# Optimization experiments

Hardware: AMD Instinct MI355X
Metric: run time of the kernel (lower is better)

## Reference

```python
import jax, jax.numpy as jnp
import numpy as np

IN_F = 4096
OUT_F = 4096
N = 16384


def setup_inputs() -> dict:
    key = jax.random.key(0)
    ks = jax.random.split(key, 7)
    return {
        "x": jax.random.normal(ks[0], (N, IN_F), dtype=jnp.float32),
        "weight_mu": jax.random.normal(ks[1], (OUT_F, IN_F), dtype=jnp.float32) * 0.1,
        "weight_rho": jax.random.normal(ks[2], (OUT_F, IN_F), dtype=jnp.float32) * 0.1,
        "bias_mu": jax.random.normal(ks[3], (OUT_F,), dtype=jnp.float32) * 0.1,
        "bias_rho": jax.random.normal(ks[4], (OUT_F,), dtype=jnp.float32) * 0.1,
        "eps_w": jax.random.normal(ks[5], (OUT_F, IN_F), dtype=jnp.float32),
        "eps_b": jax.random.normal(ks[6], (OUT_F,), dtype=jnp.float32),
    }


def reference(x, weight_mu, weight_rho, bias_mu, bias_rho, eps_w, eps_b):
    # softplus: log(1 + exp(rho)), written as log1p(exp(.)) for stability
    weight = weight_mu + jnp.log1p(jnp.exp(weight_rho)) * eps_w  # [out, in]
    bias = bias_mu + jnp.log1p(jnp.exp(bias_rho)) * eps_b        # [out]
    # F.linear(x, W, b) = x @ W.T + b
    return jnp.einsum("ni,oi->no", x, weight) + bias
```

## Files before the change

kernel.cpp:

```cpp
#include <hip/hip_runtime.h>
#include <hip/hip_bf16.h>

typedef unsigned short u16;
typedef __attribute__((ext_vector_type(4))) float f32x4;
typedef __attribute__((ext_vector_type(8))) short bf16x8;

__device__ __forceinline__ u16 f2bf(float f) {
    union { float f; unsigned u; } v; v.f = f;
    unsigned r = (v.u + 0x7fffu + ((v.u >> 16) & 1u)) >> 16;
    return (u16)r;
}

__device__ __forceinline__ float softplus(float x) {
    return (x > 15.f) ? x : log1pf(__expf(x));
}

__device__ __forceinline__ void gload_lds16(const void* g, void* l) {
    __builtin_amdgcn_global_load_lds(
        (__attribute__((address_space(1))) void*)(g),
        (__attribute__((address_space(3))) void*)(l),
        16, 0, 0);
}

#define BAR() do { asm volatile("" ::: "memory"); \
                   __builtin_amdgcn_s_barrier();  \
                   asm volatile("" ::: "memory"); } while (0)

__global__ __launch_bounds__(256) void prep_x_kernel(
        const float* __restrict__ x, u16* __restrict__ xb, int n4) {
    int i = blockIdx.x * 256 + threadIdx.x;
    if (i >= n4) return;
    float4 v = ((const float4*)x)[i];
    ushort4 o;
    o.x = f2bf(v.x); o.y = f2bf(v.y); o.z = f2bf(v.z); o.w = f2bf(v.w);
    ((ushort4*)xb)[i] = o;
}

__global__ __launch_bounds__(256) void prep_w_kernel(
        const float* __restrict__ mu, const float* __restrict__ rho,
        const float* __restrict__ eps, u16* __restrict__ wb, int n4) {
    int i = blockIdx.x * 256 + threadIdx.x;
    if (i >= n4) return;
    float4 m = ((const float4*)mu)[i];
    float4 r = ((const float4*)rho)[i];
    float4 e = ((const float4*)eps)[i];
    ushort4 o;
    o.x = f2bf(m.x + softplus(r.x) * e.x);
    o.y = f2bf(m.y + softplus(r.y) * e.y);
    o.z = f2bf(m.z + softplus(r.z) * e.z);
    o.w = f2bf(m.w + softplus(r.w) * e.w);
    ((ushort4*)wb)[i] = o;
}

__global__ __launch_bounds__(256) void prep_bias_kernel(
        const float* __restrict__ mu, const float* __restrict__ rho,
        const float* __restrict__ eps, float* __restrict__ b, int n) {
    int i = blockIdx.x * 256 + threadIdx.x;
    if (i < n) b[i] = mu[i] + softplus(rho[i]) * eps[i];
}

__device__ __forceinline__ bf16x8 ld_frag(const u16* region, int r0, int ks, int lane) {
    int row = r0 + (lane & 15);
    int kc  = (ks * 4 + (lane >> 4)) ^ (row & 7);
    return *(const bf16x8*)((const char*)region + row * 128 + kc * 16);
}

template <int MB, int NB>
__device__ __forceinline__ void mfma_quad(f32x4 (&acc)[8][4],
                                          const bf16x8 (&av)[4][2],
                                          const bf16x8 (&bv)[2][2]) {
#pragma unroll
    for (int ks = 0; ks < 2; ++ks)
#pragma unroll
        for (int mi = 0; mi < 4; ++mi)
#pragma unroll
            for (int ni = 0; ni < 2; ++ni)
                acc[MB + mi][NB + ni] = __builtin_amdgcn_mfma_f32_16x16x32_bf16(
                    av[mi][ks], bv[ni][ks], acc[MB + mi][NB + ni], 0, 0, 0);
}

#define STAGE(region, h, P, koff) do {                                          \
    gload_lds16(P[h][0] + (koff), (char*)(region) + (h) * 16384 + (w * 2 + 0) * 1024); \
    gload_lds16(P[h][1] + (koff), (char*)(region) + (h) * 16384 + (w * 2 + 1) * 1024); \
} while (0)

#define RD_A(reg, roff)                                                \
    _Pragma("unroll")                                                  \
    for (int mi = 0; mi < 4; ++mi)                                     \
        _Pragma("unroll")                                              \
        for (int ks = 0; ks < 2; ++ks)                                 \
            a[mi][ks] = ld_frag(reg, wr * 128 + (roff) + mi * 16, ks, lane)

#define RD_B(dst, reg, roff)                                           \
    _Pragma("unroll")                                                  \
    for (int ni = 0; ni < 2; ++ni)                                     \
        _Pragma("unroll")                                              \
        for (int ks = 0; ks < 2; ++ks)                                 \
            dst[ni][ks] = ld_frag(reg, wc * 64 + (roff) + ni * 16, ks, lane)

__global__ __launch_bounds__(512, 2) void gemm256_8ph(
        const u16* __restrict__ A,
        const u16* __restrict__ B,
        const float* __restrict__ bias,
        float* __restrict__ C,
        int M, int Nout, int K) {
    __shared__ __attribute__((aligned(16))) u16 smem[4][16384];
    u16* A0 = smem[0]; u16* B0 = smem[1];
    u16* A1 = smem[2]; u16* B1 = smem[3];

    const int tid  = threadIdx.x;
    const int lane = tid & 63;
    const int w    = tid >> 6;
    const int wr   = w >> 2;
    const int wc   = w & 3;

    const int nbn = Nout >> 8;
    const int nwg = (M >> 8) * nbn;
    const int cpx = nwg >> 3;
    const int swz = ((int)blockIdx.x & 7) * cpx + ((int)blockIdx.x >> 3);
    const int m0 = (swz / nbn) << 8;
    const int n0 = (swz % nbn) << 8;

    const u16* PA[2][2]; const u16* PB[2][2];
#pragma unroll
    for (int q = 0; q < 2; ++q) {
        int c   = (w * 2 + q) * 64 + lane;
        int row = c >> 3;
        int kc  = (c & 7) ^ (row & 7);
#pragma unroll
        for (int h = 0; h < 2; ++h) {
            PA[h][q] = A + (size_t)(m0 + h * 128 + row) * K + kc * 8;
            PB[h][q] = B + (size_t)(n0 + h * 128 + row) * K + kc * 8;
        }
    }

    bf16x8 a[4][2], bl[2][2], bh[2][2];
    f32x4 acc[8][4] = {};

    const int NT = K >> 6;
    const int NI = NT >> 1;

    STAGE(B0, 0, PB, 0);  STAGE(B0, 1, PB, 0);
    STAGE(A0, 0, PA, 0);  STAGE(A0, 1, PA, 0);
    STAGE(B1, 0, PB, 64); STAGE(B1, 1, PB, 64);
    STAGE(A1, 0, PA, 64);
    asm volatile("s_waitcnt vmcnt(6)" ::: "memory");
    BAR();
    RD_A(A0, 0);

#pragma unroll 1
    for (int i = 0; i < NI; ++i) {
        int t2 = 2 * i + 2; if (t2 >= NT) t2 -= NT;
        int t3 = 2 * i + 3; if (t3 >= NT) t3 -= NT;
        const int k1 = (2 * i + 1) << 6;
        const int k2 = t2 << 6;
        const int k3 = t3 << 6;

        RD_B(bl, B0, 0);
        STAGE(A1, 1, PA, k1);
        BAR();
        asm volatile("s_waitcnt lgkmcnt(0)" ::: "memory");
        __builtin_amdgcn_s_setprio(1);
        mfma_quad<0, 0>(acc, a, bl);
        __builtin_amdgcn_s_setprio(0);
        BAR();

        RD_B(bh, B0, 32);
        BAR();
        asm volatile("s_waitcnt lgkmcnt(0)" ::: "memory");
        __builtin_amdgcn_s_setprio(1);
        mfma_quad<0, 2>(acc, a, bh);
        __builtin_amdgcn_s_setprio(0);
        BAR();

        RD_A(A0, 64);
        STAGE(B0, 0, PB, k2);
        BAR();
        asm volatile("s_waitcnt lgkmcnt(0)" ::: "memory");
        __builtin_amdgcn_s_setprio(1);
        mfma_quad<4, 2>(acc, a, bh);
        __builtin_amdgcn_s_setprio(0);
        BAR();

        STAGE(B0, 1, PB, k2);
        STAGE(A0, 0, PA, k2);
        asm volatile("s_waitcnt vmcnt(6)" ::: "memory");
        BAR();
        __builtin_amdgcn_s_setprio(1);
        mfma_quad<4, 0>(acc, a, bl);
        __builtin_amdgcn_s_setprio(0);
        RD_A(A1, 0);
        BAR();

        RD_B(bl, B1, 0);
        STAGE(A0, 1, PA, k2);
        BAR();
        asm volatile("s_waitcnt lgkmcnt(0)" ::: "memory");
        __builtin_amdgcn_s_setprio(1);
        mfma_quad<0, 0>(acc, a, bl);
        __builtin_amdgcn_s_setprio(0);
        BAR();

        RD_B(bh, B1, 32);
        BAR();
        asm volatile("s_waitcnt lgkmcnt(0)" ::: "memory");
        __builtin_amdgcn_s_setprio(1);
        mfma_quad<0, 2>(acc, a, bh);
        __builtin_amdgcn_s_setprio(0);
        BAR();

        RD_A(A1, 64);
        STAGE(B1, 0, PB, k3);
        BAR();
        asm volatile("s_waitcnt lgkmcnt(0)" ::: "memory");
        __builtin_amdgcn_s_setprio(1);
        mfma_quad<4, 2>(acc, a, bh);
        __builtin_amdgcn_s_setprio(0);
        BAR();

        STAGE(B1, 1, PB, k3);
        STAGE(A1, 0, PA, k3);
        asm volatile("s_waitcnt vmcnt(6)" ::: "memory");
        BAR();
        __builtin_amdgcn_s_setprio(1);
        mfma_quad<4, 0>(acc, a, bl);
        __builtin_amdgcn_s_setprio(0);
        RD_A(A0, 0);
        BAR();
    }

    asm volatile("s_waitcnt vmcnt(0)" ::: "memory");

    const int crow = (lane >> 4) * 4;
    const int ccol = lane & 15;
#pragma unroll
    for (int mi = 0; mi < 8; ++mi) {
#pragma unroll
        for (int ni = 0; ni < 4; ++ni) {
            const int row = m0 + wr * 128 + mi * 16 + crow;
            const int col = n0 + wc * 64 + ni * 16 + ccol;
            const float bv = bias[col];
            float* Cp = C + (size_t)row * Nout + col;
#pragma unroll
            for (int q = 0; q < 4; ++q)
                Cp[(size_t)q * Nout] = acc[mi][ni][q] + bv;
        }
    }
}

extern "C" void kernel_launch(void* const* d_in, const int* in_sizes, int n_in,
                              void* d_out, int out_size, void* d_ws, size_t ws_size,
                              hipStream_t stream) {
    const float* x    = (const float*)d_in[0];
    const float* wmu  = (const float*)d_in[1];
    const float* wrho = (const float*)d_in[2];
    const float* bmu  = (const float*)d_in[3];
    const float* brho = (const float*)d_in[4];
    const float* ew   = (const float*)d_in[5];
    const float* eb   = (const float*)d_in[6];
    float* out = (float*)d_out;

    const int Nout = in_sizes[3];
    const int K    = in_sizes[1] / Nout;
    const int M    = in_sizes[0] / K;

    u16* xb = (u16*)d_ws;
    u16* wb = xb + (size_t)M * K;
    float* bs = (float*)(wb + (size_t)Nout * K);

    const int nx4 = (M * K) / 4;
    const int nw4 = (Nout * K) / 4;
    prep_x_kernel<<<(nx4 + 255) / 256, 256, 0, stream>>>(x, xb, nx4);
    prep_w_kernel<<<(nw4 + 255) / 256, 256, 0, stream>>>(wmu, wrho, ew, wb, nw4);
    prep_bias_kernel<<<(Nout + 255) / 256, 256, 0, stream>>>(bmu, brho, eb, bs, Nout);

    dim3 grid((M / 256) * (Nout / 256));
    gemm256_8ph<<<grid, 512, 0, stream>>>(xb, wb, bs, out, M, Nout, K);
}
```

Measured before the change: 571.7 us.

## Switch GEMM inner loop from 16x16x32 to 32x32x16 bf16 MFMA tiles

Replaces the 16x16x32 MFMA instruction with the 32x32x16 variant. Fragment loads, the accumulator layout, the per-phase read/compute schedule and the output store mapping are all reworked to match. The larger MFMA tile needs fewer LDS fragment reads per FLOP and fewer instruction issues. It also changes the vmcnt waits and where the A staging sits inside the 8-phase pipeline, which risks new stalls or register pressure.

Result: slower. 627.4 us (+9.7%).

```diff
diff --git a/kernel.cpp b/kernel.cpp
--- a/kernel.cpp
+++ b/kernel.cpp
@@ -2,7 +2,7 @@
 #include <hip/hip_bf16.h>
 
 typedef unsigned short u16;
-typedef __attribute__((ext_vector_type(4))) float f32x4;
+typedef __attribute__((ext_vector_type(16))) float f32x16;
 typedef __attribute__((ext_vector_type(8))) short bf16x8;
 
 __device__ __forceinline__ u16 f2bf(float f) {
@@ -59,24 +59,24 @@
     if (i < n) b[i] = mu[i] + softplus(rho[i]) * eps[i];
 }
 
-__device__ __forceinline__ bf16x8 ld_frag(const u16* region, int r0, int ks, int lane) {
-    int row = r0 + (lane & 15);
-    int kc  = (ks * 4 + (lane >> 4)) ^ (row & 7);
+__device__ __forceinline__ bf16x8 ld_frag32(const u16* region, int r0, int kc16, int lane) {
+    int row = r0 + (lane & 31);
+    int kc  = (kc16 * 2 + (lane >> 5)) ^ (row & 7);
     return *(const bf16x8*)((const char*)region + row * 128 + kc * 16);
 }
 
-template <int MB, int NB>
-__device__ __forceinline__ void mfma_quad(f32x4 (&acc)[8][4],
-                                          const bf16x8 (&av)[4][2],
-                                          const bf16x8 (&bv)[2][2]) {
-#pragma unroll
-    for (int ks = 0; ks < 2; ++ks)
-#pragma unroll
-        for (int mi = 0; mi < 4; ++mi)
+template <int MB>
+__device__ __forceinline__ void mfma8(f32x16 (&acc)[4][2],
+                                      const bf16x8 (&av)[2][2],
+                                      const bf16x8 (&bv)[2][2]) {
+#pragma unroll
+    for (int s = 0; s < 2; ++s)
+#pragma unroll
+        for (int mi = 0; mi < 2; ++mi)
 #pragma unroll
             for (int ni = 0; ni < 2; ++ni)
-                acc[MB + mi][NB + ni] = __builtin_amdgcn_mfma_f32_16x16x32_bf16(
-                    av[mi][ks], bv[ni][ks], acc[MB + mi][NB + ni], 0, 0, 0);
+                acc[MB + mi][ni] = __builtin_amdgcn_mfma_f32_32x32x16_bf16(
+                    av[mi][s], bv[ni][s], acc[MB + mi][ni], 0, 0, 0);
 }
 
 #define STAGE(region, h, P, koff) do {                                          \
@@ -84,19 +84,19 @@
     gload_lds16(P[h][1] + (koff), (char*)(region) + (h) * 16384 + (w * 2 + 1) * 1024); \
 } while (0)
 
-#define RD_A(reg, roff)                                                \
+#define RD_A32(reg, mh, kh)                                            \
     _Pragma("unroll")                                                  \
-    for (int mi = 0; mi < 4; ++mi)                                     \
+    for (int mi = 0; mi < 2; ++mi)                                     \
         _Pragma("unroll")                                              \
-        for (int ks = 0; ks < 2; ++ks)                                 \
-            a[mi][ks] = ld_frag(reg, wr * 128 + (roff) + mi * 16, ks, lane)
-
-#define RD_B(dst, reg, roff)                                           \
+        for (int s = 0; s < 2; ++s)                                    \
+            a[mi][s] = ld_frag32(reg, wr * 128 + (mh) * 64 + mi * 32, (kh) * 2 + s, lane)
+
+#define RD_B32(reg, kh)                                                \
     _Pragma("unroll")                                                  \
     for (int ni = 0; ni < 2; ++ni)                                     \
         _Pragma("unroll")                                              \
-        for (int ks = 0; ks < 2; ++ks)                                 \
-            dst[ni][ks] = ld_frag(reg, wc * 64 + (roff) + ni * 16, ks, lane)
+        for (int s = 0; s < 2; ++s)                                    \
+            bb[kh][ni][s] = ld_frag32(reg, wc * 64 + ni * 32, (kh) * 2 + s, lane)
 
 __global__ __launch_bounds__(512, 2) void gemm256_8ph(
         const u16* __restrict__ A,
@@ -134,8 +134,8 @@
         }
     }
 
-    bf16x8 a[4][2], bl[2][2], bh[2][2];
-    f32x4 acc[8][4] = {};
+    bf16x8 a[2][2], bb[2][2][2];
+    f32x16 acc[4][2] = {};
 
     const int NT = K >> 6;
     const int NI = NT >> 1;
@@ -146,7 +146,6 @@
     STAGE(A1, 0, PA, 64);
     asm volatile("s_waitcnt vmcnt(6)" ::: "memory");
     BAR();
-    RD_A(A0, 0);
 
 #pragma unroll 1
     for (int i = 0; i < NI; ++i) {
@@ -156,94 +155,102 @@
         const int k2 = t2 << 6;
         const int k3 = t3 << 6;
 
-        RD_B(bl, B0, 0);
+        RD_A32(A0, 0, 0);
+        RD_B32(B0, 0);
         STAGE(A1, 1, PA, k1);
         BAR();
         asm volatile("s_waitcnt lgkmcnt(0)" ::: "memory");
         __builtin_amdgcn_s_setprio(1);
-        mfma_quad<0, 0>(acc, a, bl);
-        __builtin_amdgcn_s_setprio(0);
-        BAR();
-
-        RD_B(bh, B0, 32);
-        BAR();
-        asm volatile("s_waitcnt lgkmcnt(0)" ::: "memory");
-        __builtin_amdgcn_s_setprio(1);
-        mfma_quad<0, 2>(acc, a, bh);
-        __builtin_amdgcn_s_setprio(0);
-        BAR();
-
-        RD_A(A0, 64);
+        mfma8<0>(acc, a, bb[0]);
+        __builtin_amdgcn_s_setprio(0);
+        BAR();
+
+        RD_A32(A0, 0, 1);
+        RD_B32(B0, 1);
+        BAR();
+        asm volatile("s_waitcnt lgkmcnt(0)" ::: "memory");
+        __builtin_amdgcn_s_setprio(1);
+        mfma8<0>(acc, a, bb[1]);
+        __builtin_amdgcn_s_setprio(0);
+        BAR();
+
+        RD_A32(A0, 1, 0);
         STAGE(B0, 0, PB, k2);
         BAR();
         asm volatile("s_waitcnt lgkmcnt(0)" ::: "memory");
         __builtin_amdgcn_s_setprio(1);
-        mfma_quad<4, 2>(acc, a, bh);
-        __builtin_amdgcn_s_setprio(0);
-        BAR();
-
+        mfma8<2>(acc, a, bb[0]);
+        __builtin_amdgcn_s_setprio(0);
+        BAR();
+
+        RD_A32(A0, 1, 1);
         STAGE(B0, 1, PB, k2);
+        asm volatile("s_waitcnt vmcnt(4)" ::: "memory");
+        BAR();
+        asm volatile("s_waitcnt lgkmcnt(0)" ::: "memory");
+        __builtin_amdgcn_s_setprio(1);
+        mfma8<2>(acc, a, bb[1]);
+        __builtin_amdgcn_s_setprio(0);
         STAGE(A0, 0, PA, k2);
-        asm volatile("s_waitcnt vmcnt(6)" ::: "memory");
-        BAR();
-        __builtin_amdgcn_s_setprio(1);
-        mfma_quad<4, 0>(acc, a, bl);
-        __builtin_amdgcn_s_setprio(0);
-        RD_A(A1, 0);
-        BAR();
-
-        RD_B(bl, B1, 0);
+        BAR();
+
+        RD_A32(A1, 0, 0);
+        RD_B32(B1, 0);
         STAGE(A0, 1, PA, k2);
         BAR();
         asm volatile("s_waitcnt lgkmcnt(0)" ::: "memory");
         __builtin_amdgcn_s_setprio(1);
-        mfma_quad<0, 0>(acc, a, bl);
-        __builtin_amdgcn_s_setprio(0);
-        BAR();
-
-        RD_B(bh, B1, 32);
-        BAR();
-        asm volatile("s_waitcnt lgkmcnt(0)" ::: "memory");
-        __builtin_amdgcn_s_setprio(1);
-        mfma_quad<0, 2>(acc, a, bh);
-        __builtin_amdgcn_s_setprio(0);
-        BAR();
-
-        RD_A(A1, 64);
+        mfma8<0>(acc, a, bb[0]);
+        __builtin_amdgcn_s_setprio(0);
+        BAR();
+
+        RD_A32(A1, 0, 1);
+        RD_B32(B1, 1);
+        BAR();
+        asm volatile("s_waitcnt lgkmcnt(0)" ::: "memory");
+        __builtin_amdgcn_s_setprio(1);
+        mfma8<0>(acc, a, bb[1]);
+        __builtin_amdgcn_s_setprio(0);
+        BAR();
+
+        RD_A32(A1, 1, 0);
         STAGE(B1, 0, PB, k3);
         BAR();
         asm volatile("s_waitcnt lgkmcnt(0)" ::: "memory");
         __builtin_amdgcn_s_setprio(1);
-        mfma_quad<4, 2>(acc, a, bh);
-        __builtin_amdgcn_s_setprio(0);
-        BAR();
-
+        mfma8<2>(acc, a, bb[0]);
+        __builtin_amdgcn_s_setprio(0);
+        BAR();
+
+        RD_A32(A1, 1, 1);
         STAGE(B1, 1, PB, k3);
+        asm volatile("s_waitcnt vmcnt(4)" ::: "memory");
+        BAR();
+        asm volatile("s_waitcnt lgkmcnt(0)" ::: "memory");
+        __builtin_amdgcn_s_setprio(1);
+        mfma8<2>(acc, a, bb[1]);
+        __builtin_amdgcn_s_setprio(0);
         STAGE(A1, 0, PA, k3);
-        asm volatile("s_waitcnt vmcnt(6)" ::: "memory");
-        BAR();
-        __builtin_amdgcn_s_setprio(1);
-        mfma_quad<4, 0>(acc, a, bl);
-        __builtin_amdgcn_s_setprio(0);
-        RD_A(A0, 0);
         BAR();
     }
 
     asm volatile("s_waitcnt vmcnt(0)" ::: "memory");
 
-    const int crow = (lane >> 4) * 4;
-    const int ccol = lane & 15;
-#pragma unroll
-    for (int mi = 0; mi < 8; ++mi) {
-#pragma unroll
-        for (int ni = 0; ni < 4; ++ni) {
-            const int row = m0 + wr * 128 + mi * 16 + crow;
-            const int col = n0 + wc * 64 + ni * 16 + ccol;
+    const int ccol = lane & 31;
+    const int crow = 4 * (lane >> 5);
+#pragma unroll
+    for (int mi = 0; mi < 4; ++mi) {
+#pragma unroll
+        for (int ni = 0; ni < 2; ++ni) {
+            const int col = n0 + wc * 64 + ni * 32 + ccol;
             const float bv = bias[col];
-            float* Cp = C + (size_t)row * Nout + col;
-#pragma unroll
-            for (int q = 0; q < 4; ++q)
-                Cp[(size_t)q * Nout] = acc[mi][ni][q] + bv;
+            const int rbase = m0 + wr * 128 + mi * 32 + crow;
+            float* Cp = C + (size_t)rbase * Nout + col;
+#pragma unroll
+            for (int reg = 0; reg < 16; ++reg) {
+                const int roff = (reg & 3) + 8 * (reg >> 2);
+                Cp[(size_t)roff * Nout] = acc[mi][ni][reg] + bv;
+            }
         }
     }
 }
```
